# Kernel tuning notes

Measured on AMD Instinct MI355X. Metric: run time of the kernel, lower is better.

Reference implementation:

```python
import jax, jax.numpy as jnp
import numpy as np


def setup_inputs() -> dict:
    key = jax.random.key(0)
    k1, k2 = jax.random.split(key)
    shape = (8, 16, 6, 256, 256)  # (n1, n2, band_num, h, w)
    inputs = jax.random.normal(k1, shape, dtype=jnp.float32)
    targets = jax.random.normal(k2, shape, dtype=jnp.float32)
    return {"inputs": inputs, "targets": targets}


def reference(inputs, targets):
    n1, n2, band_num, h, w = inputs.shape
    # Flatten to (n*band_num, h*w): each row is one band of one sample.
    x = inputs.reshape(n1 * n2 * band_num, h * w)
    y = targets.reshape(n1 * n2 * band_num, h * w)
    # torch.var uses unbiased estimator (ddof=1)
    vx = jnp.var(x, axis=1, ddof=1)
    vy = jnp.var(y, axis=1, ddof=1)
    vxy = jnp.var(x + y, axis=1, ddof=1)
    # r = 1 - 0.5*(Var(x+y) - Var(x) - Var(y)) / sqrt(|Var(x)*Var(y)|)
    r = 1.0 - 0.5 * (vxy - vx - vy) / jnp.sqrt(jnp.abs(vx * vy))
    return jnp.mean(r)
```

## Files before the change

kernel.cpp:

```cpp
#include <hip/hip_runtime.h>


#define ROWS 768
#define ROW_ELEMS 65536
#define BLOCK 256

__global__ __launch_bounds__(BLOCK) void row_r_kernel(const float* __restrict__ x,
                                                      const float* __restrict__ y,
                                                      float* __restrict__ row_r) {
    const int row = blockIdx.x;
    const float4* __restrict__ x4 = (const float4*)(x + (size_t)row * ROW_ELEMS);
    const float4* __restrict__ y4 = (const float4*)(y + (size_t)row * ROW_ELEMS);
    const int tid = threadIdx.x;

    float sx = 0.f, sy = 0.f, sxx = 0.f, syy = 0.f, sxy = 0.f;

    const int nvec = ROW_ELEMS / 4;
    for (int i = tid; i < nvec; i += BLOCK) {
        float4 a = x4[i];
        float4 b = y4[i];
        sx  += a.x + a.y + a.z + a.w;
        sy  += b.x + b.y + b.z + b.w;
        sxx += a.x*a.x + a.y*a.y + a.z*a.z + a.w*a.w;
        syy += b.x*b.x + b.y*b.y + b.z*b.z + b.w*b.w;
        sxy += a.x*b.x + a.y*b.y + a.z*b.z + a.w*b.w;
    }

    #pragma unroll
    for (int off = 32; off > 0; off >>= 1) {
        sx  += __shfl_down(sx,  off);
        sy  += __shfl_down(sy,  off);
        sxx += __shfl_down(sxx, off);
        syy += __shfl_down(syy, off);
        sxy += __shfl_down(sxy, off);
    }

    __shared__ float sm[5][BLOCK / 64];
    const int wave = tid >> 6;
    const int lane = tid & 63;
    if (lane == 0) {
        sm[0][wave] = sx;  sm[1][wave] = sy;
        sm[2][wave] = sxx; sm[3][wave] = syy;
        sm[4][wave] = sxy;
    }
    __syncthreads();

    if (tid == 0) {
        float tsx = 0.f, tsy = 0.f, tsxx = 0.f, tsyy = 0.f, tsxy = 0.f;
        #pragma unroll
        for (int w = 0; w < BLOCK / 64; ++w) {
            tsx += sm[0][w]; tsy += sm[1][w];
            tsxx += sm[2][w]; tsyy += sm[3][w];
            tsxy += sm[4][w];
        }
        const float n = (float)ROW_ELEMS;
        const float inv_nm1 = 1.0f / (n - 1.0f);
        float vx  = (tsxx - tsx * tsx / n) * inv_nm1;
        float vy  = (tsyy - tsy * tsy / n) * inv_nm1;
        float cov = (tsxy - tsx * tsy / n) * inv_nm1;
        float r = 1.0f - cov / sqrtf(fabsf(vx * vy));
        row_r[row] = r;
    }
}

__global__ __launch_bounds__(BLOCK) void mean_kernel(const float* __restrict__ row_r,
                                                     float* __restrict__ out) {
    float s = 0.f;
    for (int i = threadIdx.x; i < ROWS; i += BLOCK) s += row_r[i];

    #pragma unroll
    for (int off = 32; off > 0; off >>= 1) s += __shfl_down(s, off);

    __shared__ float sm[BLOCK / 64];
    const int wave = threadIdx.x >> 6;
    const int lane = threadIdx.x & 63;
    if (lane == 0) sm[wave] = s;
    __syncthreads();

    if (threadIdx.x == 0) {
        float t = 0.f;
        #pragma unroll
        for (int w = 0; w < BLOCK / 64; ++w) t += sm[w];
        out[0] = t / (float)ROWS;
    }
}

extern "C" void kernel_launch(void* const* d_in, const int* in_sizes, int n_in,
                              void* d_out, int out_size, void* d_ws, size_t ws_size,
                              hipStream_t stream) {
    const float* x = (const float*)d_in[0];
    const float* y = (const float*)d_in[1];
    float* row_r = (float*)d_ws;
    float* out = (float*)d_out;

    row_r_kernel<<<ROWS, BLOCK, 0, stream>>>(x, y, row_r);
    mean_kernel<<<1, BLOCK, 0, stream>>>(row_r, out);
}
```

Before: 390.7 us.

## Split each row across blocks and unroll loads for more memory parallelism

```diff
diff --git a/kernel.cpp b/kernel.cpp
--- a/kernel.cpp
+++ b/kernel.cpp
@@ -4,26 +4,51 @@
 #define ROWS 768
 #define ROW_ELEMS 65536
 #define BLOCK 256
+#define SPLIT 4
+#define NBLK (ROWS * SPLIT)
+#define CHUNK_VECS (ROW_ELEMS / 4 / SPLIT)
 
-__global__ __launch_bounds__(BLOCK) void row_r_kernel(const float* __restrict__ x,
-                                                      const float* __restrict__ y,
-                                                      float* __restrict__ row_r) {
-    const int row = blockIdx.x;
-    const float4* __restrict__ x4 = (const float4*)(x + (size_t)row * ROW_ELEMS);
-    const float4* __restrict__ y4 = (const float4*)(y + (size_t)row * ROW_ELEMS);
+__global__ __launch_bounds__(BLOCK) void partial_kernel(const float* __restrict__ x,
+                                                        const float* __restrict__ y,
+                                                        float* __restrict__ part) {
+    const int blk = blockIdx.x;
+    const int row = blk / SPLIT;
+    const int chunk = blk % SPLIT;
+    const size_t base = (size_t)row * ROW_ELEMS + (size_t)chunk * (ROW_ELEMS / SPLIT);
+    const float4* __restrict__ x4 = (const float4*)(x + base);
+    const float4* __restrict__ y4 = (const float4*)(y + base);
     const int tid = threadIdx.x;
 
     float sx = 0.f, sy = 0.f, sxx = 0.f, syy = 0.f, sxy = 0.f;
 
-    const int nvec = ROW_ELEMS / 4;
-    for (int i = tid; i < nvec; i += BLOCK) {
-        float4 a = x4[i];
-        float4 b = y4[i];
-        sx  += a.x + a.y + a.z + a.w;
-        sy  += b.x + b.y + b.z + b.w;
-        sxx += a.x*a.x + a.y*a.y + a.z*a.z + a.w*a.w;
-        syy += b.x*b.x + b.y*b.y + b.z*b.z + b.w*b.w;
-        sxy += a.x*b.x + a.y*b.y + a.z*b.z + a.w*b.w;
+    #pragma unroll
+    for (int base_i = 0; base_i < 4; ++base_i) {
+        const int i = tid + base_i * (BLOCK * 4);
+        float4 a0 = x4[i];
+        float4 a1 = x4[i + BLOCK];
+        float4 a2 = x4[i + BLOCK * 2];
+        float4 a3 = x4[i + BLOCK * 3];
+        float4 b0 = y4[i];
+        float4 b1 = y4[i + BLOCK];
+        float4 b2 = y4[i + BLOCK * 2];
+        float4 b3 = y4[i + BLOCK * 3];
+
+        sx  += (a0.x + a0.y + a0.z + a0.w) + (a1.x + a1.y + a1.z + a1.w)
+             + (a2.x + a2.y + a2.z + a2.w) + (a3.x + a3.y + a3.z + a3.w);
+        sy  += (b0.x + b0.y + b0.z + b0.w) + (b1.x + b1.y + b1.z + b1.w)
+             + (b2.x + b2.y + b2.z + b2.w) + (b3.x + b3.y + b3.z + b3.w);
+        sxx += a0.x*a0.x + a0.y*a0.y + a0.z*a0.z + a0.w*a0.w
+             + a1.x*a1.x + a1.y*a1.y + a1.z*a1.z + a1.w*a1.w
+             + a2.x*a2.x + a2.y*a2.y + a2.z*a2.z + a2.w*a2.w
+             + a3.x*a3.x + a3.y*a3.y + a3.z*a3.z + a3.w*a3.w;
+        syy += b0.x*b0.x + b0.y*b0.y + b0.z*b0.z + b0.w*b0.w
+             + b1.x*b1.x + b1.y*b1.y + b1.z*b1.z + b1.w*b1.w
+             + b2.x*b2.x + b2.y*b2.y + b2.z*b2.z + b2.w*b2.w
+             + b3.x*b3.x + b3.y*b3.y + b3.z*b3.z + b3.w*b3.w;
+        sxy += a0.x*b0.x + a0.y*b0.y + a0.z*b0.z + a0.w*b0.w
+             + a1.x*b1.x + a1.y*b1.y + a1.z*b1.z + a1.w*b1.w
+             + a2.x*b2.x + a2.y*b2.y + a2.z*b2.z + a2.w*b2.w
+             + a3.x*b3.x + a3.y*b3.y + a3.z*b3.z + a3.w*b3.w;
     }
 
     #pragma unroll
@@ -46,35 +71,50 @@
     __syncthreads();
 
     if (tid == 0) {
+        float t0 = 0.f, t1 = 0.f, t2 = 0.f, t3 = 0.f, t4 = 0.f;
+        #pragma unroll
+        for (int w = 0; w < BLOCK / 64; ++w) {
+            t0 += sm[0][w]; t1 += sm[1][w];
+            t2 += sm[2][w]; t3 += sm[3][w];
+            t4 += sm[4][w];
+        }
+        part[0 * NBLK + blk] = t0;
+        part[1 * NBLK + blk] = t1;
+        part[2 * NBLK + blk] = t2;
+        part[3 * NBLK + blk] = t3;
+        part[4 * NBLK + blk] = t4;
+    }
+}
+
+__global__ __launch_bounds__(BLOCK) void finalize_kernel(const float* __restrict__ part,
+                                                         float* __restrict__ out) {
+    float acc = 0.f;
+    for (int row = threadIdx.x; row < ROWS; row += BLOCK) {
         float tsx = 0.f, tsy = 0.f, tsxx = 0.f, tsyy = 0.f, tsxy = 0.f;
         #pragma unroll
-        for (int w = 0; w < BLOCK / 64; ++w) {
-            tsx += sm[0][w]; tsy += sm[1][w];
-            tsxx += sm[2][w]; tsyy += sm[3][w];
-            tsxy += sm[4][w];
+        for (int c = 0; c < SPLIT; ++c) {
+            const int b = row * SPLIT + c;
+            tsx  += part[0 * NBLK + b];
+            tsy  += part[1 * NBLK + b];
+            tsxx += part[2 * NBLK + b];
+            tsyy += part[3 * NBLK + b];
+            tsxy += part[4 * NBLK + b];
         }
         const float n = (float)ROW_ELEMS;
         const float inv_nm1 = 1.0f / (n - 1.0f);
         float vx  = (tsxx - tsx * tsx / n) * inv_nm1;
         float vy  = (tsyy - tsy * tsy / n) * inv_nm1;
         float cov = (tsxy - tsx * tsy / n) * inv_nm1;
-        float r = 1.0f - cov / sqrtf(fabsf(vx * vy));
-        row_r[row] = r;
+        acc += 1.0f - cov / sqrtf(fabsf(vx * vy));
     }
-}
-
-__global__ __launch_bounds__(BLOCK) void mean_kernel(const float* __restrict__ row_r,
-                                                     float* __restrict__ out) {
-    float s = 0.f;
-    for (int i = threadIdx.x; i < ROWS; i += BLOCK) s += row_r[i];
 
     #pragma unroll
-    for (int off = 32; off > 0; off >>= 1) s += __shfl_down(s, off);
+    for (int off = 32; off > 0; off >>= 1) acc += __shfl_down(acc, off);
 
     __shared__ float sm[BLOCK / 64];
     const int wave = threadIdx.x >> 6;
     const int lane = threadIdx.x & 63;
-    if (lane == 0) sm[wave] = s;
+    if (lane == 0) sm[wave] = acc;
     __syncthreads();
 
     if (threadIdx.x == 0) {
@@ -90,9 +130,9 @@
                               hipStream_t stream) {
     const float* x = (const float*)d_in[0];
     const float* y = (const float*)d_in[1];
-    float* row_r = (float*)d_ws;
+    float* part = (float*)d_ws;
     float* out = (float*)d_out;
 
-    row_r_kernel<<<ROWS, BLOCK, 0, stream>>>(x, y, row_r);
-    mean_kernel<<<1, BLOCK, 0, stream>>>(row_r, out);
+    partial_kernel<<<NBLK, BLOCK, 0, stream>>>(x, y, part);
+    finalize_kernel<<<1, BLOCK, 0, stream>>>(part, out);
 }
```

Result: no change. 388.6 us (-0.5%).
